# Performance work log

Hardware: AMD Instinct MI355X
Metric: run time of the kernel (lower is better)

The kernel has to match this reference:

```python
import jax, jax.numpy as jnp
import numpy as np

B, S, D, H = 4, 2048, 1024, 16
HD = D // H  # 64


def setup_inputs() -> dict:
    key = jax.random.key(0)
    ks = jax.random.split(key, 9)
    s = 1.0 / np.sqrt(D)
    return {
        "x": jax.random.normal(ks[0], (B, S, D), dtype=jnp.float32),
        "Wq": jax.random.normal(ks[1], (D, D), dtype=jnp.float32) * s,
        "bq": jax.random.normal(ks[2], (D,), dtype=jnp.float32) * 0.01,
        "Wk": jax.random.normal(ks[3], (D, D), dtype=jnp.float32) * s,
        "bk": jax.random.normal(ks[4], (D,), dtype=jnp.float32) * 0.01,
        "Wv": jax.random.normal(ks[5], (D, D), dtype=jnp.float32) * s,
        "bv": jax.random.normal(ks[6], (D,), dtype=jnp.float32) * 0.01,
        "Wo": jax.random.normal(ks[7], (D, D), dtype=jnp.float32) * s,
        "bo": jax.random.normal(ks[8], (D,), dtype=jnp.float32) * 0.01,
    }


def reference(x, Wq, bq, Wk, bk, Wv, bv, Wo, bo):
    b, s, _ = x.shape
    # projections -> [b, h, s, hd]
    def proj(W, bias):
        return (x @ W.T + bias).reshape(b, s, H, HD).transpose(0, 2, 1, 3)
    q, k, v = proj(Wq, bq), proj(Wk, bk), proj(Wv, bv)
    # NOTE: source multiplies by sqrt(head_dim)**0.5 = head_dim**0.25 (quirk kept)
    scale = jnp.asarray(HD, dtype=x.dtype) ** 0.25
    scores = jnp.einsum("bhqd,bhkd->bhqk", q, k) * scale
    causal = jnp.tril(jnp.ones((s, s), dtype=bool))
    scores = jnp.where(causal, scores, -jnp.inf)
    attn = jax.nn.softmax(scores, axis=-1)  # dropout p=0 (eval) -> identity
    out = jnp.einsum("bhqk,bhkd->bhqd", attn, v)
    out = out.transpose(0, 2, 1, 3).reshape(b, s, D)
    return out @ Wo.T + bo
```

## Files before the change

### kernel.cpp

```cpp
#include <hip/hip_runtime.h>
#include <hip/hip_fp16.h>


typedef unsigned short u16;
typedef unsigned int u32;
typedef _Float16 half8 __attribute__((ext_vector_type(8)));
typedef float f32x4 __attribute__((ext_vector_type(4)));
typedef unsigned short ushort8 __attribute__((ext_vector_type(8)));
typedef unsigned short us4 __attribute__((ext_vector_type(4)));
typedef unsigned int u32x2 __attribute__((ext_vector_type(2)));

#define SCL2 4.0816663172343815f
#define SWZ(r) ((((r) ^ ((r) >> 3))) & 7)

__device__ __forceinline__ u16 f2h(float f) {
  return __half_as_ushort(__float2half(f));
}

__device__ __forceinline__ us4 pack4(float a, float b, float c, float d) {
  u32x2 t;
  t[0] = __builtin_bit_cast(u32, __builtin_amdgcn_cvt_pkrtz(a, b));
  t[1] = __builtin_bit_cast(u32, __builtin_amdgcn_cvt_pkrtz(c, d));
  return __builtin_bit_cast(us4, t);
}

__device__ __forceinline__ void gload16(const void* gsrc, void* ldst) {
  typedef __attribute__((address_space(1))) const void glob_t;
  typedef __attribute__((address_space(3))) void lds_t;
  __builtin_amdgcn_global_load_lds((glob_t*)gsrc, (lds_t*)ldst, 16, 0, 0);
}

__device__ __forceinline__ f32x4 mfma_f16(half8 a, half8 b, f32x4 c) {
  return __builtin_amdgcn_mfma_f32_16x16x32_f16(a, b, c, 0, 0, 0);
}

__global__ __launch_bounds__(256) void cvt_f32_f16(const float* __restrict__ in,
                                                   u16* __restrict__ out, int n8) {
  int i = blockIdx.x * 256 + threadIdx.x;
  if (i >= n8) return;
  const float4* p = (const float4*)in + (size_t)i * 2;
  float4 a = p[0], b = p[1];
  ushort8 v;
  v[0] = f2h(a.x); v[1] = f2h(a.y); v[2] = f2h(a.z); v[3] = f2h(a.w);
  v[4] = f2h(b.x); v[5] = f2h(b.y); v[6] = f2h(b.z); v[7] = f2h(b.w);
  *(ushort8*)(out + (size_t)i * 8) = v;
}

__device__ __forceinline__ void gemm_body(const u16* __restrict__ A, const u16* __restrict__ Bw,
                                          const float* __restrict__ bias,
                                          u16* __restrict__ Ch, float* __restrict__ Cf,
                                          u16* __restrict__ Vtp) {
  __shared__ __align__(16) u16 sA[128 * 32];
  __shared__ __align__(16) u16 sB[128 * 32];
  const int m0 = blockIdx.y * 128, n0 = blockIdx.x * 128;
  const int tid = threadIdx.x, w = tid >> 6, l = tid & 63;
  const int wm = (w >> 1) * 64, wn = (w & 1) * 64;
  f32x4 acc[4][4] = {};
  const int srow = tid >> 2, sch = (tid & 3) * 8;
  char* sAb = (char*)sA + w * 1024;
  char* sBb = (char*)sB + w * 1024;
  const u16* Ag0 = A + (size_t)(m0 + srow) * 1024 + sch;
  const u16* Ag1 = A + (size_t)(m0 + 64 + srow) * 1024 + sch;
  const u16* Bg0 = Bw + (size_t)(n0 + srow) * 1024 + sch;
  const u16* Bg1 = Bw + (size_t)(n0 + 64 + srow) * 1024 + sch;
  for (int kt = 0; kt < 32; ++kt) {
    const int k0 = kt * 32;
    __syncthreads();
    gload16(Ag0 + k0, sAb);
    gload16(Ag1 + k0, sAb + 4096);
    gload16(Bg0 + k0, sBb);
    gload16(Bg1 + k0, sBb + 4096);
    __syncthreads();
    half8 a[4], b[4];
#pragma unroll
    for (int mf = 0; mf < 4; ++mf)
      a[mf] = *(const half8*)&sA[(wm + mf * 16 + (l & 15)) * 32 + (l >> 4) * 8];
#pragma unroll
    for (int nf = 0; nf < 4; ++nf)
      b[nf] = *(const half8*)&sB[(wn + nf * 16 + (l & 15)) * 32 + (l >> 4) * 8];
#pragma unroll
    for (int mf = 0; mf < 4; ++mf)
#pragma unroll
      for (int nf = 0; nf < 4; ++nf)
        acc[mf][nf] = mfma_f16(a[mf], b[nf], acc[mf][nf]);
  }
  if (Vtp) {
#pragma unroll
    for (int nf = 0; nf < 4; ++nf) {
      const int col = n0 + wn + nf * 16 + (l & 15);
      const float bv = bias[col];
#pragma unroll
      for (int mf = 0; mf < 4; ++mf) {
        const int row = m0 + wm + mf * 16 + (l >> 4) * 4;
        us4 v;
#pragma unroll
        for (int r = 0; r < 4; ++r) v[r] = f2h(acc[mf][nf][r] + bv);
        *(us4*)(Vtp + (size_t)((row >> 11) * 16 + (col >> 6)) * 131072 +
                (size_t)(col & 63) * 2048 + (row & 2047)) = v;
      }
    }
  } else {
#pragma unroll
    for (int nf = 0; nf < 4; ++nf) {
      const int col = n0 + wn + nf * 16 + (l & 15);
      const float bv = bias[col];
#pragma unroll
      for (int mf = 0; mf < 4; ++mf) {
#pragma unroll
        for (int r = 0; r < 4; ++r) {
          const int row = m0 + wm + mf * 16 + (l >> 4) * 4 + r;
          float v = acc[mf][nf][r] + bv;
          if (Cf) Cf[(size_t)row * 1024 + col] = v;
          else    Ch[(size_t)row * 1024 + col] = f2h(v);
        }
      }
    }
  }
}

struct QkvArgs {
  const u16* B[3];
  const float* bias[3];
  u16* C[3];
};

__global__ __launch_bounds__(256) void gemm_qkv(const u16* __restrict__ A, QkvArgs ga) {
  const int z = blockIdx.z;
  if (z == 2) gemm_body(A, ga.B[2], ga.bias[2], nullptr, nullptr, ga.C[2]);
  else        gemm_body(A, ga.B[z], ga.bias[z], ga.C[z], nullptr, nullptr);
}

__global__ __launch_bounds__(256) void gemm_out(const u16* __restrict__ A, const u16* __restrict__ Bw,
                                                const float* __restrict__ bias, float* __restrict__ C) {
  gemm_body(A, Bw, bias, nullptr, C, nullptr);
}

__global__ __launch_bounds__(256) void attn_fused(const u16* __restrict__ Qb, const u16* __restrict__ Kb,
                                                  const u16* __restrict__ Vt, u16* __restrict__ Ob) {
  __shared__ __align__(16) u16 k_s[2 * 64 * 64];
  __shared__ __align__(16) u16 vt_s[2 * 64 * 64];
  __shared__ __align__(16) u16 p_s[4 * 16 * 64];
  const int bid = blockIdx.x;
  const int bh = bid & 63;
  const int pj = bid >> 6;
  const int b = bh >> 4, h = bh & 15;
  const size_t baseQ = (size_t)b * 2048 * 1024 + h * 64;
  const size_t baseV = (size_t)(b * 16 + h) * 131072;
  const int tid = threadIdx.x, w = tid >> 6, l = tid & 63;
  const int g = l >> 4, qi = l & 15;
  const int q_loc = w * 16 + qi;

  const int srow = w * 8 + (l >> 3);
  const int sch0 = (l & 7) ^ SWZ(srow);
  const int sch1 = (l & 7) ^ SWZ(srow + 32);
  int koff[4], pvoff[2], voff[4][2];
#pragma unroll
  for (int nf = 0; nf < 4; ++nf) {
    const int row = nf * 16 + qi;
    koff[nf] = row * 64 + ((g ^ SWZ(row)) << 3);
#pragma unroll
    for (int ks = 0; ks < 2; ++ks)
      voff[nf][ks] = row * 64 + (((ks * 4 + g) ^ SWZ(row)) << 3);
  }
#pragma unroll
  for (int ks = 0; ks < 2; ++ks)
    pvoff[ks] = qi * 64 + (((ks * 4 + g) ^ SWZ(qi)) << 3);
  u16* pw = p_s + w * 1024;

  const u16* pK0;
  const u16* pK1;
  const u16* pV0;
  const u16* pV1;
  auto stage = [&](int buf) {
    char* kb = (char*)k_s + buf * 8192;
    char* vb = (char*)vt_s + buf * 8192;
    gload16(pK0, kb + w * 1024);
    gload16(pK1, kb + 4096 + w * 1024);
    gload16(pV0, vb + w * 1024);
    gload16(pV1, vb + 4096 + w * 1024);
    pK0 += 65536; pK1 += 65536; pV0 += 64; pV1 += 64;
  };

  int cur = 0;
  for (int half = 0; half < 2; ++half) {
    const int qt = half ? (31 - pj) : pj;
    const int q0 = qt * 64;
    const int q_glob = q0 + q_loc;

    half8 qf0, qf1;
    {
      const u16* qp = Qb + baseQ + (size_t)q_glob * 1024 + g * 8;
      qf0 = *(const half8*)(qp);
      qf1 = *(const half8*)(qp + 32);
    }
    pK0 = Kb + baseQ + (size_t)srow * 1024 + sch0 * 8;
    pK1 = Kb + baseQ + (size_t)(srow + 32) * 1024 + sch1 * 8;
    pV0 = Vt + baseV + (size_t)srow * 2048 + sch0 * 8;
    pV1 = Vt + baseV + (size_t)(srow + 32) * 2048 + sch1 * 8;

    f32x4 s[4], o[4] = {};
    float m_r = -INFINITY, l_r = 0.f;

    stage(cur);
    __syncthreads();

    for (int kt = 0; kt <= qt; ++kt) {
      if (kt < qt) stage(cur ^ 1);
      const u16* kbuf = k_s + cur * 4096;
      const u16* vbuf = vt_s + cur * 4096;
#pragma unroll
      for (int nf = 0; nf < 4; ++nf) {
        half8 k0 = *(const half8*)(kbuf + koff[nf]);
        half8 k1 = *(const half8*)(kbuf + (koff[nf] ^ 32));
        f32x4 acc = {};
        acc = mfma_f16(k0, qf0, acc);
        acc = mfma_f16(k1, qf1, acc);
        s[nf] = acc * SCL2;
      }
      if (kt == qt) {
#pragma unroll
        for (int nf = 0; nf < 4; ++nf) {
          const int kb = nf * 16 + g * 4;
#pragma unroll
          for (int r = 0; r < 4; ++r)
            if (kb + r > q_loc) s[nf][r] = -INFINITY;
        }
      }
      float t = fmaxf(fmaxf(fmaxf(s[0][0], s[0][1]), s[0][2]),
                      fmaxf(fmaxf(s[0][3], s[1][0]), s[1][1]));
      t = fmaxf(t, fmaxf(fmaxf(s[1][2], s[1][3]), s[2][0]));
      t = fmaxf(t, fmaxf(fmaxf(s[2][1], s[2][2]), s[2][3]));
      t = fmaxf(t, fmaxf(fmaxf(s[3][0], s[3][1]), s[3][2]));
      t = fmaxf(t, s[3][3]);
      t = fmaxf(t, __shfl_xor(t, 16));
      t = fmaxf(t, __shfl_xor(t, 32));
      if (!__all(t <= m_r + 8.f)) {
        const float mn = fmaxf(m_r, t);
        const float al = __builtin_amdgcn_exp2f(m_r - mn);
        l_r *= al;
#pragma unroll
        for (int nf = 0; nf < 4; ++nf) o[nf] *= al;
        m_r = mn;
      }
      float rs = 0.f;
#pragma unroll
      for (int nf = 0; nf < 4; ++nf) {
#pragma unroll
        for (int r = 0; r < 4; ++r) {
          const float p = __builtin_amdgcn_exp2f(s[nf][r] - m_r);
          s[nf][r] = p;
          rs += p;
        }
      }
      rs += __shfl_xor(rs, 16);
      rs += __shfl_xor(rs, 32);
      l_r += rs;
#pragma unroll
      for (int nf = 0; nf < 4; ++nf) {
        const int c = nf * 2 + (g >> 1);
        *(us4*)(pw + qi * 64 + ((c ^ SWZ(qi)) << 3) + (g & 1) * 4) =
            pack4(s[nf][0], s[nf][1], s[nf][2], s[nf][3]);
      }
#pragma unroll
      for (int ks = 0; ks < 2; ++ks) {
        half8 pf = *(const half8*)(pw + pvoff[ks]);
#pragma unroll
        for (int nf = 0; nf < 4; ++nf) {
          half8 vf = *(const half8*)(vbuf + voff[nf][ks]);
          o[nf] = mfma_f16(vf, pf, o[nf]);
        }
      }
      __syncthreads();
      cur ^= 1;
    }
    const float inv = 1.f / l_r;
    u16* op = Ob + (size_t)(b * 2048 + q_glob) * 1024 + h * 64 + g * 4;
#pragma unroll
    for (int nf = 0; nf < 4; ++nf)
      *(us4*)(op + nf * 16) =
          pack4(o[nf][0] * inv, o[nf][1] * inv, o[nf][2] * inv, o[nf][3] * inv);
  }
}

extern "C" void kernel_launch(void* const* d_in, const int* in_sizes, int n_in,
                              void* d_out, int out_size, void* d_ws, size_t ws_size,
                              hipStream_t stream) {
  (void)in_sizes; (void)n_in; (void)out_size; (void)ws_size;
  const float* x  = (const float*)d_in[0];
  const float* Wq = (const float*)d_in[1];
  const float* bq = (const float*)d_in[2];
  const float* Wk = (const float*)d_in[3];
  const float* bk = (const float*)d_in[4];
  const float* Wv = (const float*)d_in[5];
  const float* bv = (const float*)d_in[6];
  const float* Wo = (const float*)d_in[7];
  const float* bo = (const float*)d_in[8];

  u16* xb = (u16*)d_ws;
  u16* wq = xb + (size_t)8192 * 1024;
  u16* wk = wq + 1024 * 1024;
  u16* wv = wk + 1024 * 1024;
  u16* wo = wv + 1024 * 1024;
  u16* Qb = wo + 1024 * 1024;
  u16* Kb = Qb + (size_t)8192 * 1024;
  u16* Vt = Kb + (size_t)8192 * 1024;
  u16* Ab = xb;

  cvt_f32_f16<<<4096, 256, 0, stream>>>(x, xb, 1048576);
  cvt_f32_f16<<<512, 256, 0, stream>>>(Wq, wq, 131072);
  cvt_f32_f16<<<512, 256, 0, stream>>>(Wk, wk, 131072);
  cvt_f32_f16<<<512, 256, 0, stream>>>(Wv, wv, 131072);
  cvt_f32_f16<<<512, 256, 0, stream>>>(Wo, wo, 131072);

  QkvArgs ga;
  ga.B[0] = wq; ga.B[1] = wk; ga.B[2] = wv;
  ga.bias[0] = bq; ga.bias[1] = bk; ga.bias[2] = bv;
  ga.C[0] = Qb; ga.C[1] = Kb; ga.C[2] = Vt;
  gemm_qkv<<<dim3(8, 64, 3), 256, 0, stream>>>(xb, ga);

  attn_fused<<<1024, 256, 0, stream>>>(Qb, Kb, Vt, Ab);

  gemm_out<<<dim3(8, 64), 256, 0, stream>>>(Ab, wo, bo, (float*)d_out);
}
```

Measured before the change: 296.3 us.

## Double-buffer GEMM LDS tiles, swizzle LDS layout, remap blocks for XCD locality

The GEMM main loop now uses two LDS buffers, so the next K-tile is loaded while MFMAs run on the current one, and only one barrier is needed per iteration instead of two. The global-to-LDS column chunk is XOR-swizzled by row to reduce LDS bank conflicts on the fragment reads. Grid launches become 1D, with a remap that spreads consecutive block IDs across the 8 XCDs so that blocks sharing an M-row land on the same die for L2 reuse. The cost is double the LDS per block, which may lower occupancy.

```diff
diff --git a/kernel.cpp b/kernel.cpp
--- a/kernel.cpp
+++ b/kernel.cpp
@@ -49,40 +49,46 @@
 __device__ __forceinline__ void gemm_body(const u16* __restrict__ A, const u16* __restrict__ Bw,
                                           const float* __restrict__ bias,
                                           u16* __restrict__ Ch, float* __restrict__ Cf,
-                                          u16* __restrict__ Vtp) {
-  __shared__ __align__(16) u16 sA[128 * 32];
-  __shared__ __align__(16) u16 sB[128 * 32];
-  const int m0 = blockIdx.y * 128, n0 = blockIdx.x * 128;
+                                          u16* __restrict__ Vtp, int m0, int n0) {
+  __shared__ __align__(16) u16 sA[2][128 * 32];
+  __shared__ __align__(16) u16 sB[2][128 * 32];
   const int tid = threadIdx.x, w = tid >> 6, l = tid & 63;
   const int wm = (w >> 1) * 64, wn = (w & 1) * 64;
   f32x4 acc[4][4] = {};
-  const int srow = tid >> 2, sch = (tid & 3) * 8;
-  char* sAb = (char*)sA + w * 1024;
-  char* sBb = (char*)sB + w * 1024;
+  const int srow = tid >> 2;
+  const int sch = ((tid & 3) ^ ((srow >> 1) & 3)) * 8;
   const u16* Ag0 = A + (size_t)(m0 + srow) * 1024 + sch;
   const u16* Ag1 = A + (size_t)(m0 + 64 + srow) * 1024 + sch;
   const u16* Bg0 = Bw + (size_t)(n0 + srow) * 1024 + sch;
   const u16* Bg1 = Bw + (size_t)(n0 + 64 + srow) * 1024 + sch;
+  auto stage = [&](int buf, int k0) {
+    char* a = (char*)sA[buf] + w * 1024;
+    char* b = (char*)sB[buf] + w * 1024;
+    gload16(Ag0 + k0, a);
+    gload16(Ag1 + k0, a + 4096);
+    gload16(Bg0 + k0, b);
+    gload16(Bg1 + k0, b + 4096);
+  };
+  stage(0, 0);
+  __syncthreads();
+  int cur = 0;
+  const int ca = ((l >> 4) ^ (((l & 15) >> 1) & 3)) * 8;
   for (int kt = 0; kt < 32; ++kt) {
-    const int k0 = kt * 32;
-    __syncthreads();
-    gload16(Ag0 + k0, sAb);
-    gload16(Ag1 + k0, sAb + 4096);
-    gload16(Bg0 + k0, sBb);
-    gload16(Bg1 + k0, sBb + 4096);
-    __syncthreads();
+    if (kt < 31) stage(cur ^ 1, (kt + 1) * 32);
     half8 a[4], b[4];
 #pragma unroll
     for (int mf = 0; mf < 4; ++mf)
-      a[mf] = *(const half8*)&sA[(wm + mf * 16 + (l & 15)) * 32 + (l >> 4) * 8];
+      a[mf] = *(const half8*)&sA[cur][(wm + mf * 16 + (l & 15)) * 32 + ca];
 #pragma unroll
     for (int nf = 0; nf < 4; ++nf)
-      b[nf] = *(const half8*)&sB[(wn + nf * 16 + (l & 15)) * 32 + (l >> 4) * 8];
+      b[nf] = *(const half8*)&sB[cur][(wn + nf * 16 + (l & 15)) * 32 + ca];
 #pragma unroll
     for (int mf = 0; mf < 4; ++mf)
 #pragma unroll
       for (int nf = 0; nf < 4; ++nf)
         acc[mf][nf] = mfma_f16(a[mf], b[nf], acc[mf][nf]);
+    __syncthreads();
+    cur ^= 1;
   }
   if (Vtp) {
 #pragma unroll
@@ -125,14 +131,21 @@
 };
 
 __global__ __launch_bounds__(256) void gemm_qkv(const u16* __restrict__ A, QkvArgs ga) {
-  const int z = blockIdx.z;
-  if (z == 2) gemm_body(A, ga.B[2], ga.bias[2], nullptr, nullptr, ga.C[2]);
-  else        gemm_body(A, ga.B[z], ga.bias[z], ga.C[z], nullptr, nullptr);
+  const int lin = blockIdx.x;
+  const int wid = (lin & 7) * 192 + (lin >> 3);
+  const int mblk = wid / 24;
+  const int rem = wid - mblk * 24;
+  const int z = rem >> 3, nblk = rem & 7;
+  if (z == 2) gemm_body(A, ga.B[2], ga.bias[2], nullptr, nullptr, ga.C[2], mblk * 128, nblk * 128);
+  else        gemm_body(A, ga.B[z], ga.bias[z], ga.C[z], nullptr, nullptr, mblk * 128, nblk * 128);
 }
 
 __global__ __launch_bounds__(256) void gemm_out(const u16* __restrict__ A, const u16* __restrict__ Bw,
                                                 const float* __restrict__ bias, float* __restrict__ C) {
-  gemm_body(A, Bw, bias, nullptr, C, nullptr);
+  const int lin = blockIdx.x;
+  const int wid = (lin & 7) * 64 + (lin >> 3);
+  const int mblk = wid >> 3, nblk = wid & 7;
+  gemm_body(A, Bw, bias, nullptr, C, nullptr, mblk * 128, nblk * 128);
 }
 
 __global__ __launch_bounds__(256) void attn_fused(const u16* __restrict__ Qb, const u16* __restrict__ Kb,
@@ -316,9 +329,9 @@
   ga.B[0] = wq; ga.B[1] = wk; ga.B[2] = wv;
   ga.bias[0] = bq; ga.bias[1] = bk; ga.bias[2] = bv;
   ga.C[0] = Qb; ga.C[1] = Kb; ga.C[2] = Vt;
-  gemm_qkv<<<dim3(8, 64, 3), 256, 0, stream>>>(xb, ga);
+  gemm_qkv<<<1536, 256, 0, stream>>>(xb, ga);
 
   attn_fused<<<1024, 256, 0, stream>>>(Qb, Kb, Vt, Ab);
 
-  gemm_out<<<dim3(8, 64), 256, 0, stream>>>(Ab, wo, bo, (float*)d_out);
-}
+  gemm_out<<<512, 256, 0, stream>>>(Ab, wo, bo, (float*)d_out);
+}
```

Result: no change. 297.8 us (+0.5%).
